# Optimization experiments

Hardware: AMD Instinct MI355X
Metric: run time of the kernel (lower is better)

## Reference

```python
import jax, jax.numpy as jnp
import numpy as np

B, N, E = 16, 1024, 32768
HEADS, OC = 4, 8          # GATConv: out_channels = d_out // heads = 8
D_IN, A_DIM = 33, 8
DM, DO = 16, 32
EPS_LN = 1e-5


def setup_inputs() -> dict:
    key = jax.random.key(0)
    ks = jax.random.split(key, 24)
    r = lambda k, s: (0.1 * jax.random.normal(k, s)).astype(jnp.float32)
    return {
        "H": jax.random.normal(ks[0], (B, N, D_IN + A_DIM + 1), dtype=jnp.float32),
        "edge_index": jax.random.randint(ks[1], (2, E), 0, N, dtype=jnp.int32),
        "fc_s_w": r(ks[2], (DM, D_IN)), "fc_s_b": r(ks[3], (DM,)),
        "fc_a_w": r(ks[4], (DM, A_DIM)), "fc_a_b": r(ks[5], (DM,)),
        "fc_r_w": r(ks[6], (DM, 1)), "fc_r_b": r(ks[7], (DM,)),
        "fuse_q": r(ks[8], (3, DM)),
        "fuse_k_w": r(ks[9], (DM, DM)),
        "fuse_v_w": r(ks[10], (DM, DM)),
        "proj_w": r(ks[11], (DO, DM)), "proj_b": r(ks[12], (DO,)),
        "post_w": r(ks[13], (DO, DO)), "post_b": r(ks[14], (DO,)),
        "ln_g": jnp.ones((DO,), jnp.float32), "ln_b": jnp.zeros((DO,), jnp.float32),
        "gat_w": r(ks[15], (HEADS * OC, DO)),
        "att_src": r(ks[16], (HEADS, OC)),
        "att_dst": r(ks[17], (HEADS, OC)),
        "gat_b": r(ks[18], (HEADS * OC,)),
    }


def reference(H, edge_index, fc_s_w, fc_s_b, fc_a_w, fc_a_b, fc_r_w, fc_r_b,
              fuse_q, fuse_k_w, fuse_v_w, proj_w, proj_b, post_w, post_b,
              ln_g, ln_b, gat_w, att_src, att_dst, gat_b):
    # ---- ObsEmbedding: split obs | prev-action | prev-reward, embed to DM ----
    s = H[..., :D_IN]
    a = H[..., D_IN:D_IN + A_DIM]
    rr = H[..., D_IN + A_DIM:]
    tok = jnp.stack([s @ fc_s_w.T + fc_s_b,
                     a @ fc_a_w.T + fc_a_b,
                     rr @ fc_r_w.T + fc_r_b], axis=-2)            # [B,N,3,DM]
    K = tok @ fuse_k_w.T
    V = tok @ fuse_v_w.T
    attn = jnp.einsum('qd,bntd->bnqt', fuse_q, K) / jnp.sqrt(jnp.float32(DM))
    w = jax.nn.softmax(attn, axis=-1)                             # [B,N,3,3]
    fused = jnp.einsum('bnqt,bntd->bnqd', w, V).mean(-2)          # [B,N,DM]
    z = jax.nn.relu(fused) @ proj_w.T + proj_b                    # [B,N,DO]
    h = jax.nn.relu(z @ post_w.T + post_b)
    mu = h.mean(-1, keepdims=True)
    var = ((h - mu) ** 2).mean(-1, keepdims=True)
    Hn = (h - mu) / jnp.sqrt(var + EPS_LN) * ln_g + ln_b          # [B,N,DO]

    # ---- GATConv (eval mode: dropout off, add_self_loops=False) ----
    src, dst = edge_index[0], edge_index[1]
    x = (Hn @ gat_w.T).reshape(B, N, HEADS, OC)                   # [B,N,H,OC]
    a_s = (x * att_src).sum(-1)                                   # [B,N,H]
    a_d = (x * att_dst).sum(-1)
    e = jax.nn.leaky_relu(a_s[:, src] + a_d[:, dst], 0.2)         # [B,E,H]

    def per_graph(e_b, x_b):
        # scatter-softmax over incoming edges of each destination node
        m = jax.ops.segment_max(e_b, dst, num_segments=N)
        ex = jnp.exp(e_b - m[dst])
        den = jax.ops.segment_sum(ex, dst, num_segments=N)
        alpha = ex / den[dst]                                     # [E,H]
        out = jax.ops.segment_sum(alpha[:, :, None] * x_b[src], dst,
                                  num_segments=N)                 # [N,H,OC]
        A = jnp.zeros((HEADS, N, N), jnp.float32).at[:, src, dst].add(alpha.T)
        A = A / jnp.maximum(A.sum(-1, keepdims=True), 1e-9)
        return out.reshape(N, HEADS * OC) + gat_b, A

    out, A = jax.vmap(per_graph)(e, x)                            # [B,N,32], [B,H,N,N]
    return out, A
```

## Files before the change

kernel.cpp:

```cpp
#include <hip/hip_runtime.h>
#include <math.h>

namespace {

constexpr int B = 16, N = 1024, E = 32768, HEADS = 4, OC = 8;
constexpr int D_IN = 33, A_DIM = 8, DM = 16, DO = 32;
constexpr int F = D_IN + A_DIM + 1;
constexpr int BCAP = 256;
constexpr int LCAP = 128;
constexpr int FILLB = E / 256;
constexpr int ROWS_PER_BLK = 8;

typedef float f4 __attribute__((ext_vector_type(4)));
typedef float f2 __attribute__((ext_vector_type(2)));

__device__ __forceinline__ float lrelu(float x) { return x >= 0.f ? x : 0.2f * x; }


__global__ __launch_bounds__(256) void k_prep(
    const int* __restrict__ ei, int* __restrict__ cnt_src,
    int* __restrict__ cnt_dst, int* __restrict__ bkt_src,
    int* __restrict__ bkt_dst,
    const float* __restrict__ H,
    const float* __restrict__ fc_s_w, const float* __restrict__ fc_s_b,
    const float* __restrict__ fc_a_w, const float* __restrict__ fc_a_b,
    const float* __restrict__ fc_r_w, const float* __restrict__ fc_r_b,
    const float* __restrict__ fuse_q, const float* __restrict__ fuse_k_w,
    const float* __restrict__ fuse_v_w, const float* __restrict__ proj_w,
    const float* __restrict__ proj_b, const float* __restrict__ post_w,
    const float* __restrict__ post_b, const float* __restrict__ ln_g,
    const float* __restrict__ ln_b, const float* __restrict__ gat_w,
    const float* __restrict__ att_src, const float* __restrict__ att_dst,
    float* __restrict__ x_out, float* __restrict__ as_out, float* __restrict__ advi) {
  if (blockIdx.x < FILLB) {
    int e = blockIdx.x * 256 + threadIdx.x;
    int s = ei[e], d = ei[E + e];
    int p1 = atomicAdd(&cnt_src[s], 1);
    if (p1 < BCAP) bkt_src[s * BCAP + p1] = d;
    int p2 = atomicAdd(&cnt_dst[d], 1);
    if (p2 < BCAP) bkt_dst[d * BCAP + p2] = s;
    return;
  }
  int node = (blockIdx.x - FILLB) * 256 + threadIdx.x;
  if (node >= B * N) return;

  const float* hin = H + (size_t)node * F;
  float hv[F];
#pragma unroll
  for (int i = 0; i < F; i++) hv[i] = hin[i];

  float tok[3][DM];
#pragma unroll
  for (int j = 0; j < DM; j++) {
    float acc = fc_s_b[j];
#pragma unroll
    for (int i = 0; i < D_IN; i++) acc = fmaf(hv[i], fc_s_w[j * D_IN + i], acc);
    tok[0][j] = acc;
    float acc2 = fc_a_b[j];
#pragma unroll
    for (int i = 0; i < A_DIM; i++) acc2 = fmaf(hv[D_IN + i], fc_a_w[j * A_DIM + i], acc2);
    tok[1][j] = acc2;
    tok[2][j] = fmaf(hv[F - 1], fc_r_w[j], fc_r_b[j]);
  }

  float Kf[3][DM], Vf[3][DM];
#pragma unroll
  for (int t = 0; t < 3; t++) {
#pragma unroll
    for (int j = 0; j < DM; j++) {
      float ak = 0.f, av = 0.f;
#pragma unroll
      for (int d = 0; d < DM; d++) {
        ak = fmaf(tok[t][d], fuse_k_w[j * DM + d], ak);
        av = fmaf(tok[t][d], fuse_v_w[j * DM + d], av);
      }
      Kf[t][j] = ak; Vf[t][j] = av;
    }
  }

  float wbar[3] = {0.f, 0.f, 0.f};
#pragma unroll
  for (int q = 0; q < 3; q++) {
    float att[3];
#pragma unroll
    for (int t = 0; t < 3; t++) {
      float acc = 0.f;
#pragma unroll
      for (int d = 0; d < DM; d++) acc = fmaf(fuse_q[q * DM + d], Kf[t][d], acc);
      att[t] = acc * 0.25f;
    }
    float mx = fmaxf(att[0], fmaxf(att[1], att[2]));
    float e0 = expf(att[0] - mx), e1 = expf(att[1] - mx), e2 = expf(att[2] - mx);
    float inv = 1.f / (e0 + e1 + e2);
    wbar[0] += e0 * inv; wbar[1] += e1 * inv; wbar[2] += e2 * inv;
  }

  float fused[DM];
#pragma unroll
  for (int d = 0; d < DM; d++) {
    float f = (wbar[0] * Vf[0][d] + wbar[1] * Vf[1][d] + wbar[2] * Vf[2][d]) * (1.f / 3.f);
    fused[d] = fmaxf(f, 0.f);
  }

  float z[DO];
#pragma unroll
  for (int o = 0; o < DO; o++) {
    float acc = proj_b[o];
#pragma unroll
    for (int d = 0; d < DM; d++) acc = fmaf(fused[d], proj_w[o * DM + d], acc);
    z[o] = acc;
  }

  float h2[DO]; float mu = 0.f;
#pragma unroll
  for (int o = 0; o < DO; o++) {
    float acc = post_b[o];
#pragma unroll
    for (int d = 0; d < DO; d++) acc = fmaf(z[d], post_w[o * DO + d], acc);
    acc = fmaxf(acc, 0.f);
    h2[o] = acc; mu += acc;
  }
  mu *= (1.f / DO);
  float var = 0.f;
#pragma unroll
  for (int o = 0; o < DO; o++) { float dd = h2[o] - mu; var = fmaf(dd, dd, var); }
  var *= (1.f / DO);
  float rstd = rsqrtf(var + 1e-5f);
  float Hn[DO];
#pragma unroll
  for (int o = 0; o < DO; o++) Hn[o] = fmaf((h2[o] - mu) * rstd, ln_g[o], ln_b[o]);

  float* xrow = x_out + (size_t)node * (HEADS * OC);
  f4 asv;
#pragma unroll
  for (int hh = 0; hh < HEADS; hh++) {
    float as = 0.f, ad = 0.f;
#pragma unroll
    for (int oc = 0; oc < OC; oc++) {
      int k = hh * OC + oc;
      float acc = 0.f;
#pragma unroll
      for (int d = 0; d < DO; d++) acc = fmaf(Hn[d], gat_w[k * DO + d], acc);
      xrow[k] = acc;
      as = fmaf(acc, att_src[k], as);
      ad = fmaf(acc, att_dst[k], ad);
    }
    asv[hh] = as;
    advi[(size_t)node * 8 + 2 * hh] = ad;
  }
  *(f4*)(as_out + (size_t)node * HEADS) = asv;
}

__global__ __launch_bounds__(256) void k_inv(
    const int* __restrict__ cnt_dst, const int* __restrict__ bkt_dst,
    const float* __restrict__ as_, float* __restrict__ advi) {
  int w = threadIdx.x >> 6, lane = threadIdx.x & 63;
  int r = blockIdx.x * 4 + w;
  int b = r & (B - 1), dn = r >> 4;
  int deg = min(cnt_dst[dn], BCAP);
  const int* list = bkt_dst + dn * BCAP;

  const float* adp = advi + (size_t)(b * N + dn) * 8;
  float a0 = adp[0], a1 = adp[2], a2 = adp[4], a3 = adp[6];

  float sm0 = 0.f, sm1 = 0.f, sm2 = 0.f, sm3 = 0.f;
  for (int i = lane; i < deg; i += 64) {
    int s = list[i];
    f4 ap = *(const f4*)(as_ + (size_t)(b * N + s) * HEADS);
    sm0 += __expf(lrelu(ap.x + a0));
    sm1 += __expf(lrelu(ap.y + a1));
    sm2 += __expf(lrelu(ap.z + a2));
    sm3 += __expf(lrelu(ap.w + a3));
  }
#pragma unroll
  for (int off = 1; off < 64; off <<= 1) {
    sm0 += __shfl_xor(sm0, off);
    sm1 += __shfl_xor(sm1, off);
    sm2 += __shfl_xor(sm2, off);
    sm3 += __shfl_xor(sm3, off);
  }
  if (lane == 0) {
    float* ivp = advi + (size_t)(b * N + dn) * 8 + 1;
    ivp[0] = sm0 > 0.f ? 1.f / sm0 : 0.f;
    ivp[2] = sm1 > 0.f ? 1.f / sm1 : 0.f;
    ivp[4] = sm2 > 0.f ? 1.f / sm2 : 0.f;
    ivp[6] = sm3 > 0.f ? 1.f / sm3 : 0.f;
  }
}

__global__ __launch_bounds__(256) void k_outA(
    const int* __restrict__ cnt_src, const int* __restrict__ bkt_src,
    const int* __restrict__ cnt_dst, const int* __restrict__ bkt_dst,
    const float* __restrict__ as_, const float* __restrict__ advi,
    const float* __restrict__ x_, const float* __restrict__ gat_b,
    float* __restrict__ out, float* __restrict__ A) {
  __shared__ float row[HEADS][N];
  __shared__ int l_listO[LCAP], l_listI[LCAP];
  int h = threadIdx.x >> 6, lane = threadIdx.x & 63;
  f4* rowv = (f4*)row[h];

  int r0 = blockIdx.x * ROWS_PER_BLK;
  int s = r0 >> 4;
  int degO = min(cnt_src[s], BCAP);
  const int* listO = bkt_src + s * BCAP;
  int degI = min(cnt_dst[s], BCAP);
  const int* listI = bkt_dst + s * BCAP;
  float gb = gat_b[h * OC + (lane & 7)];

  for (int i = threadIdx.x; i < LCAP; i += 256) {
    if (i < degO) l_listO[i] = listO[i];
    if (i < degI) l_listI[i] = listI[i];
  }
  __syncthreads();

  for (int r = r0; r < r0 + ROWS_PER_BLK; ++r) {
    int b = r & (B - 1);

#pragma unroll
    for (int j = 0; j < 4; j++) rowv[lane + j * 64] = (f4){0.f, 0.f, 0.f, 0.f};
    __syncthreads();

    float as_h = as_[(size_t)(b * N + s) * HEADS + h];
    float rs = 0.f;
    for (int i = lane; i < degO; i += 64) {
      int d = (i < LCAP) ? l_listO[i] : listO[i];
      f2 rec = *(const f2*)(advi + (size_t)(b * N + d) * 8 + 2 * h);
      float a = __expf(lrelu(as_h + rec.x)) * rec.y;
      atomicAdd(&row[h][d], a);
      rs += a;
    }
#pragma unroll
    for (int off = 1; off < 64; off <<= 1) rs += __shfl_xor(rs, off);

    {
      f2 self = *(const f2*)(advi + (size_t)(b * N + s) * 8 + 2 * h);
      int eslot = lane >> 3, cl = lane & 7, c = h * OC + cl;
      float acc = 0.f;
      for (int i = eslot; i < degI; i += 8) {
        int src = (i < LCAP) ? l_listI[i] : listI[i];
        float ex = __expf(lrelu(as_[(size_t)(b * N + src) * HEADS + h] + self.x));
        acc = fmaf(ex, x_[(size_t)(b * N + src) * (HEADS * OC) + c], acc);
      }
      acc += __shfl_xor(acc, 8);
      acc += __shfl_xor(acc, 16);
      acc += __shfl_xor(acc, 32);
      if (eslot == 0)
        out[(size_t)(b * N + s) * (HEADS * OC) + c] = acc * self.y + gb;
    }

    __syncthreads();

    float ivr = 1.f / fmaxf(rs, 1e-9f);
    float* Arow = A + (((size_t)b * HEADS + h) * N + s) * N;
#pragma unroll
    for (int j = 0; j < 4; j++) {
      f4 v = rowv[lane + j * 64];
      v.x *= ivr; v.y *= ivr; v.z *= ivr; v.w *= ivr;
      __builtin_nontemporal_store(v, (f4*)Arow + lane + j * 64);
    }
  }
}

}

extern "C" void kernel_launch(void* const* d_in, const int* in_sizes, int n_in,
                              void* d_out, int out_size, void* d_ws, size_t ws_size,
                              hipStream_t stream) {
  const float* H      = (const float*)d_in[0];
  const int*   ei     = (const int*)  d_in[1];
  const float* fc_s_w = (const float*)d_in[2];
  const float* fc_s_b = (const float*)d_in[3];
  const float* fc_a_w = (const float*)d_in[4];
  const float* fc_a_b = (const float*)d_in[5];
  const float* fc_r_w = (const float*)d_in[6];
  const float* fc_r_b = (const float*)d_in[7];
  const float* fuse_q = (const float*)d_in[8];
  const float* fuse_k_w = (const float*)d_in[9];
  const float* fuse_v_w = (const float*)d_in[10];
  const float* proj_w = (const float*)d_in[11];
  const float* proj_b = (const float*)d_in[12];
  const float* post_w = (const float*)d_in[13];
  const float* post_b = (const float*)d_in[14];
  const float* ln_g   = (const float*)d_in[15];
  const float* ln_b   = (const float*)d_in[16];
  const float* gat_w  = (const float*)d_in[17];
  const float* att_src = (const float*)d_in[18];
  const float* att_dst = (const float*)d_in[19];
  const float* gat_b  = (const float*)d_in[20];

  float* out = (float*)d_out;
  float* A   = out + (size_t)B * N * DO;

  float* ws   = (float*)d_ws;
  float* xbuf = ws;
  float* asb  = xbuf + (size_t)B * N * (HEADS * OC);
  float* advi = asb + (size_t)B * N * HEADS;
  int* ibase   = (int*)(advi + (size_t)B * N * 8);
  int* cnt_src = ibase;
  int* cnt_dst = cnt_src + N;
  int* bkt_src = cnt_dst + N;
  int* bkt_dst = bkt_src + N * BCAP;

  (void)hipMemsetAsync(cnt_src, 0, 2 * N * sizeof(int), stream);
  k_prep<<<dim3(FILLB + (B * N) / 256), dim3(256), 0, stream>>>(
      ei, cnt_src, cnt_dst, bkt_src, bkt_dst,
      H, fc_s_w, fc_s_b, fc_a_w, fc_a_b, fc_r_w, fc_r_b, fuse_q, fuse_k_w,
      fuse_v_w, proj_w, proj_b, post_w, post_b, ln_g, ln_b, gat_w, att_src,
      att_dst, xbuf, asb, advi);

  k_inv<<<dim3(B * N / 4), dim3(256), 0, stream>>>(cnt_dst, bkt_dst, asb, advi);

  k_outA<<<dim3(B * N / ROWS_PER_BLK), dim3(256), 0, stream>>>(
      cnt_src, bkt_src, cnt_dst, bkt_dst, asb, advi, xbuf, gat_b, out, A);
}
```

Baseline: 106.0 us.

## Move GAT node-output aggregation into the denominator kernel, reusing cached exp values

Moves the per-destination weighted aggregation of x into the kernel that computes the softmax denominators. The exp values and source indices are cached in shared memory (up to 96 edges per destination) so they are not recomputed. This leaves the A-matrix kernel with only the row scatter and normalisation, which shortens its per-row critical path. The cost is extra shared memory and work in the first kernel, plus a fallback path that recomputes exp for destinations with more than 96 incoming edges.

New measurement: 121.4 us. 14.5% more time.

```diff
diff --git a/kernel.cpp b/kernel.cpp
--- a/kernel.cpp
+++ b/kernel.cpp
@@ -8,6 +8,7 @@
 constexpr int F = D_IN + A_DIM + 1;
 constexpr int BCAP = 256;
 constexpr int LCAP = 128;
+constexpr int XCAP = 96;
 constexpr int FILLB = E / 256;
 constexpr int ROWS_PER_BLK = 8;
 
@@ -151,9 +152,13 @@
   *(f4*)(as_out + (size_t)node * HEADS) = asv;
 }
 
-__global__ __launch_bounds__(256) void k_inv(
+__global__ __launch_bounds__(256) void k_dstf(
     const int* __restrict__ cnt_dst, const int* __restrict__ bkt_dst,
-    const float* __restrict__ as_, float* __restrict__ advi) {
+    const float* __restrict__ as_, float* __restrict__ advi,
+    const float* __restrict__ x_, const float* __restrict__ gat_b,
+    float* __restrict__ out) {
+  __shared__ f4 s_ex[4][XCAP];
+  __shared__ int s_src[4][XCAP];
   int w = threadIdx.x >> 6, lane = threadIdx.x & 63;
   int r = blockIdx.x * 4 + w;
   int b = r & (B - 1), dn = r >> 4;
@@ -167,10 +172,13 @@
   for (int i = lane; i < deg; i += 64) {
     int s = list[i];
     f4 ap = *(const f4*)(as_ + (size_t)(b * N + s) * HEADS);
-    sm0 += __expf(lrelu(ap.x + a0));
-    sm1 += __expf(lrelu(ap.y + a1));
-    sm2 += __expf(lrelu(ap.z + a2));
-    sm3 += __expf(lrelu(ap.w + a3));
+    f4 ex;
+    ex.x = __expf(lrelu(ap.x + a0));
+    ex.y = __expf(lrelu(ap.y + a1));
+    ex.z = __expf(lrelu(ap.z + a2));
+    ex.w = __expf(lrelu(ap.w + a3));
+    if (i < XCAP) { s_src[w][i] = s; s_ex[w][i] = ex; }
+    sm0 += ex.x; sm1 += ex.y; sm2 += ex.z; sm3 += ex.w;
   }
 #pragma unroll
   for (int off = 1; off < 64; off <<= 1) {
@@ -179,23 +187,42 @@
     sm2 += __shfl_xor(sm2, off);
     sm3 += __shfl_xor(sm3, off);
   }
+  float iv0 = sm0 > 0.f ? 1.f / sm0 : 0.f;
+  float iv1 = sm1 > 0.f ? 1.f / sm1 : 0.f;
+  float iv2 = sm2 > 0.f ? 1.f / sm2 : 0.f;
+  float iv3 = sm3 > 0.f ? 1.f / sm3 : 0.f;
   if (lane == 0) {
     float* ivp = advi + (size_t)(b * N + dn) * 8 + 1;
-    ivp[0] = sm0 > 0.f ? 1.f / sm0 : 0.f;
-    ivp[2] = sm1 > 0.f ? 1.f / sm1 : 0.f;
-    ivp[4] = sm2 > 0.f ? 1.f / sm2 : 0.f;
-    ivp[6] = sm3 > 0.f ? 1.f / sm3 : 0.f;
-  }
-}
-
-__global__ __launch_bounds__(256) void k_outA(
+    ivp[0] = iv0; ivp[2] = iv1; ivp[4] = iv2; ivp[6] = iv3;
+  }
+
+  int c = lane & 31, eslot = lane >> 5;
+  int h3 = c >> 3;
+  float ih  = h3 == 0 ? iv0 : h3 == 1 ? iv1 : h3 == 2 ? iv2 : iv3;
+  float adh = h3 == 0 ? a0  : h3 == 1 ? a1  : h3 == 2 ? a2  : a3;
+  float acc = 0.f;
+  for (int i = eslot; i < deg; i += 2) {
+    float exv; int src;
+    if (i < XCAP) {
+      src = s_src[w][i];
+      exv = s_ex[w][i][h3];
+    } else {
+      src = list[i];
+      exv = __expf(lrelu(as_[(size_t)(b * N + src) * HEADS + h3] + adh));
+    }
+    acc = fmaf(exv, x_[(size_t)(b * N + src) * (HEADS * OC) + c], acc);
+  }
+  acc += __shfl_xor(acc, 32);
+  if (lane < 32)
+    out[(size_t)(b * N + dn) * (HEADS * OC) + c] = acc * ih + gat_b[c];
+}
+
+__global__ __launch_bounds__(256) void k_A(
     const int* __restrict__ cnt_src, const int* __restrict__ bkt_src,
-    const int* __restrict__ cnt_dst, const int* __restrict__ bkt_dst,
     const float* __restrict__ as_, const float* __restrict__ advi,
-    const float* __restrict__ x_, const float* __restrict__ gat_b,
-    float* __restrict__ out, float* __restrict__ A) {
+    float* __restrict__ A) {
   __shared__ float row[HEADS][N];
-  __shared__ int l_listO[LCAP], l_listI[LCAP];
+  __shared__ int l_listO[LCAP];
   int h = threadIdx.x >> 6, lane = threadIdx.x & 63;
   f4* rowv = (f4*)row[h];
 
@@ -203,14 +230,9 @@
   int s = r0 >> 4;
   int degO = min(cnt_src[s], BCAP);
   const int* listO = bkt_src + s * BCAP;
-  int degI = min(cnt_dst[s], BCAP);
-  const int* listI = bkt_dst + s * BCAP;
-  float gb = gat_b[h * OC + (lane & 7)];
-
-  for (int i = threadIdx.x; i < LCAP; i += 256) {
+
+  for (int i = threadIdx.x; i < LCAP; i += 256)
     if (i < degO) l_listO[i] = listO[i];
-    if (i < degI) l_listI[i] = listI[i];
-  }
   __syncthreads();
 
   for (int r = r0; r < r0 + ROWS_PER_BLK; ++r) {
@@ -231,22 +253,6 @@
     }
 #pragma unroll
     for (int off = 1; off < 64; off <<= 1) rs += __shfl_xor(rs, off);
-
-    {
-      f2 self = *(const f2*)(advi + (size_t)(b * N + s) * 8 + 2 * h);
-      int eslot = lane >> 3, cl = lane & 7, c = h * OC + cl;
-      float acc = 0.f;
-      for (int i = eslot; i < degI; i += 8) {
-        int src = (i < LCAP) ? l_listI[i] : listI[i];
-        float ex = __expf(lrelu(as_[(size_t)(b * N + src) * HEADS + h] + self.x));
-        acc = fmaf(ex, x_[(size_t)(b * N + src) * (HEADS * OC) + c], acc);
-      }
-      acc += __shfl_xor(acc, 8);
-      acc += __shfl_xor(acc, 16);
-      acc += __shfl_xor(acc, 32);
-      if (eslot == 0)
-        out[(size_t)(b * N + s) * (HEADS * OC) + c] = acc * self.y + gb;
-    }
 
     __syncthreads();
 
@@ -308,8 +314,9 @@
       fuse_v_w, proj_w, proj_b, post_w, post_b, ln_g, ln_b, gat_w, att_src,
       att_dst, xbuf, asb, advi);
 
-  k_inv<<<dim3(B * N / 4), dim3(256), 0, stream>>>(cnt_dst, bkt_dst, asb, advi);
-
-  k_outA<<<dim3(B * N / ROWS_PER_BLK), dim3(256), 0, stream>>>(
-      cnt_src, bkt_src, cnt_dst, bkt_dst, asb, advi, xbuf, gat_b, out, A);
-}
+  k_dstf<<<dim3(B * N / 4), dim3(256), 0, stream>>>(cnt_dst, bkt_dst, asb, advi,
+                                                    xbuf, gat_b, out);
+
+  k_A<<<dim3(B * N / ROWS_PER_BLK), dim3(256), 0, stream>>>(
+      cnt_src, bkt_src, asb, advi, A);
+}
```
